# Optimization experiments

Hardware: AMD Instinct MI355X
Metric: run time of the kernel (lower is better)

The kernel has to match this reference:

```python
import jax, jax.numpy as jnp
import numpy as np

N_NODES = 100000
C = 128
E = 800000
V = 50000
NEG_SLOPE = 0.2


def gat_conv(x, edges, W, att_src, att_dst, bias, num_nodes):
    """Single-head PyG-style GATConv with self-loops added (PyG default).

    edges: [2, E] with row 0 = source j, row 1 = destination i.
    """
    loops = jnp.arange(num_nodes, dtype=edges.dtype)
    src = jnp.concatenate([edges[0], loops])  # [E+N]
    dst = jnp.concatenate([edges[1], loops])

    h = x @ W.T                               # [N, C] linear transform
    a_s = h @ att_src                         # [N] per-node src score
    a_d = h @ att_dst                         # [N] per-node dst score

    e = jax.nn.leaky_relu(a_s[src] + a_d[dst], NEG_SLOPE)  # [E+N]
    # scatter-softmax over edges grouped by destination node
    m = jax.ops.segment_max(e, dst, num_segments=num_nodes)
    ex = jnp.exp(e - m[dst])
    denom = jax.ops.segment_sum(ex, dst, num_segments=num_nodes)
    alpha = ex / (denom[dst] + 1e-16)         # [E+N]

    out = jax.ops.segment_sum(alpha[:, None] * h[src], dst, num_segments=num_nodes)
    return out + bias


def setup_inputs() -> dict:
    key = jax.random.key(0)
    ks = jax.random.split(key, 12)
    s = 1.0 / np.sqrt(C)
    return {
        "embedding": jax.random.normal(ks[0], (N_NODES, C), jnp.float32),
        "W1": jax.random.normal(ks[1], (C, C), jnp.float32) * s,
        "att_src1": jax.random.normal(ks[2], (C,), jnp.float32) * s,
        "att_dst1": jax.random.normal(ks[3], (C,), jnp.float32) * s,
        "b1": jax.random.normal(ks[4], (C,), jnp.float32) * s,
        "W2": jax.random.normal(ks[5], (C, C), jnp.float32) * s,
        "att_src2": jax.random.normal(ks[6], (C,), jnp.float32) * s,
        "att_dst2": jax.random.normal(ks[7], (C,), jnp.float32) * s,
        "b2": jax.random.normal(ks[8], (C,), jnp.float32) * s,
        "edges1": jax.random.randint(ks[9], (2, E), 0, N_NODES, jnp.int64 if jax.config.jax_enable_x64 else jnp.int32),
        "edges2": jax.random.randint(ks[10], (2, E), 0, N_NODES, jnp.int64 if jax.config.jax_enable_x64 else jnp.int32),
        "idx_mapping": jax.random.randint(ks[11], (V,), 0, N_NODES, jnp.int64 if jax.config.jax_enable_x64 else jnp.int32),
    }


def reference(embedding, W1, att_src1, att_dst1, b1, W2, att_src2, att_dst2, b2,
              edges1, edges2, idx_mapping):
    h = gat_conv(embedding, edges1, W1, att_src1, att_dst1, b1, N_NODES)
    h = gat_conv(h, edges2, W2, att_src2, att_dst2, b2, N_NODES)
    return h[idx_mapping]
```

## Files before the change

### kernel.cpp

```cpp
#include <hip/hip_runtime.h>

#define N_NODES 100000
#define C_DIM 128
#define E_EDGES 800000
#define V_OUT 50000
#define EN (E_EDGES + N_NODES)
#define M2 (2 * N_NODES)
#define EN2 (2 * EN)

#define BSHIFT 9
#define NBUCK_L ((N_NODES + 511) >> 9)
#define NBUCK2 (2 * NBUCK_L)
#define CAP 8192
#define P1_CHUNK 4096
#define P1_PER_T (P1_CHUNK / 256)
#define NCHUNK ((EN2 + P1_CHUNK - 1) / P1_CHUNK)

#define XPAD 136
#define LDS_E 768

typedef unsigned int uint;
typedef unsigned short ushort;
typedef __attribute__((ext_vector_type(8))) short bf16x8;
typedef __attribute__((ext_vector_type(4))) float f32x4;

static __device__ __forceinline__ ushort f2bf(float f) {
    uint u = __float_as_uint(f);
    u += 0x7fffu + ((u >> 16) & 1);
    return (ushort)(u >> 16);
}

#define PREP_WBLK (C_DIM * C_DIM / 4 / 256)
#define PREP_VBLK ((V_OUT + 255) / 256)
__global__ void prep_kernel(const float* __restrict__ W1, const float* __restrict__ W2,
                            ushort* __restrict__ W1b, ushort* __restrict__ W2b,
                            const int* __restrict__ idx, int* __restrict__ vflag)
{
    const int b = blockIdx.x;
    if (b < 2 * PREP_WBLK) {
        const float* in  = (b < PREP_WBLK) ? W1 : W2;
        ushort* outp     = (b < PREP_WBLK) ? W1b : W2b;
        int i = (b % PREP_WBLK) * 256 + threadIdx.x;
        float4 v = reinterpret_cast<const float4*>(in)[i];
        ushort4 r;
        r.x = f2bf(v.x); r.y = f2bf(v.y); r.z = f2bf(v.z); r.w = f2bf(v.w);
        reinterpret_cast<ushort4*>(outp)[i] = r;
    } else {
        int v = (b - 2 * PREP_WBLK) * 256 + threadIdx.x;
        if (v < V_OUT) vflag[idx[v]] = 1;
    }
}

template <int IN_F32>
__global__ __launch_bounds__(256) void gemm_mfma(
    const void* __restrict__ xin, const ushort* __restrict__ Wb,
    const float* __restrict__ att_s, const float* __restrict__ att_d,
    ushort* __restrict__ hb, float* __restrict__ a_s, float* __restrict__ a_d)
{
    __shared__ ushort xs[64 * XPAD];
    __shared__ ushort ws[128 * XPAD];
    const int tid = threadIdx.x;
    const int nb = blockIdx.x * 64;

    {
        const int row = tid >> 2, q = tid & 3;
        const long srow = min(nb + row, N_NODES - 1);
        ushort* dst = &xs[row * XPAD + q * 32];
        if (IN_F32) {
            const float* src = (const float*)xin + srow * 128 + q * 32;
            #pragma unroll
            for (int i = 0; i < 4; ++i) {
                float4 u = *reinterpret_cast<const float4*>(src + i * 8);
                float4 v = *reinterpret_cast<const float4*>(src + i * 8 + 4);
                uint4 pk;
                pk.x = (uint)f2bf(u.x) | ((uint)f2bf(u.y) << 16);
                pk.y = (uint)f2bf(u.z) | ((uint)f2bf(u.w) << 16);
                pk.z = (uint)f2bf(v.x) | ((uint)f2bf(v.y) << 16);
                pk.w = (uint)f2bf(v.z) | ((uint)f2bf(v.w) << 16);
                *reinterpret_cast<uint4*>(dst + i * 8) = pk;
            }
        } else {
            const ushort* src = (const ushort*)xin + srow * 128 + q * 32;
            #pragma unroll
            for (int i = 0; i < 4; ++i)
                *reinterpret_cast<uint4*>(dst + i * 8) =
                    *reinterpret_cast<const uint4*>(src + i * 8);
        }
    }
    {
        const int row = tid >> 1, half = tid & 1;
        const ushort* src = Wb + row * 128 + half * 64;
        ushort* dst = &ws[row * XPAD + half * 64];
        #pragma unroll
        for (int i = 0; i < 8; ++i)
            *reinterpret_cast<uint4*>(dst + i * 8) =
                *reinterpret_cast<const uint4*>(src + i * 8);
    }
    __syncthreads();

    const int lane = tid & 63;
    const int wv   = tid >> 6;
    const int n0   = nb + wv * 16;
    if (n0 >= N_NODES) return;
    const int m    = lane & 15;
    const int quad = lane >> 4;

    bf16x8 a[4];
    #pragma unroll
    for (int ki = 0; ki < 4; ++ki)
        a[ki] = *reinterpret_cast<const bf16x8*>(&xs[(wv * 16 + m) * XPAD + quad * 8 + ki * 32]);

    float ps[4] = {0, 0, 0, 0}, pd[4] = {0, 0, 0, 0};

    #pragma unroll
    for (int ct = 0; ct < 8; ++ct) {
        const int c = ct * 16 + m;
        f32x4 acc = {0.f, 0.f, 0.f, 0.f};
        #pragma unroll
        for (int ki = 0; ki < 4; ++ki) {
            bf16x8 b = *reinterpret_cast<const bf16x8*>(&ws[c * XPAD + quad * 8 + ki * 32]);
            acc = __builtin_amdgcn_mfma_f32_16x16x32_bf16(a[ki], b, acc, 0, 0, 0);
        }
        const float asc = att_s[c], adc = att_d[c];
        #pragma unroll
        for (int r = 0; r < 4; ++r) {
            const int node = n0 + quad * 4 + r;
            hb[(long)node * 128 + c] = f2bf(acc[r]);
            ps[r] = fmaf(acc[r], asc, ps[r]);
            pd[r] = fmaf(acc[r], adc, pd[r]);
        }
    }
    #pragma unroll
    for (int r = 0; r < 4; ++r) {
        float s = ps[r], d = pd[r];
        #pragma unroll
        for (int x = 1; x < 16; x <<= 1) { s += __shfl_xor(s, x); d += __shfl_xor(d, x); }
        if (m == 0) {
            const int node = n0 + quad * 4 + r;
            a_s[node] = s; a_d[node] = d;
        }
    }
}

__global__ __launch_bounds__(256) void partition_kernel(
    const int* __restrict__ e1, const int* __restrict__ e2,
    int* __restrict__ cursor, uint* __restrict__ slab)
{
    __shared__ int cnt[NBUCK2];
    __shared__ int basearr[NBUCK2];
    const int tid = threadIdx.x;
    for (int i = tid; i < NBUCK2; i += 256) cnt[i] = 0;
    __syncthreads();

    const int e0 = blockIdx.x * P1_CHUNK;
    uint ent[P1_PER_T];
    int  bkt[P1_PER_T];
    #pragma unroll
    for (int i = 0; i < P1_PER_T; ++i) {
        int e = e0 + i * 256 + tid;
        bkt[i] = -1;
        if (e < EN2) {
            int src, dst, lb;
            if (e < EN) {
                if (e < E_EDGES) { src = e1[e]; dst = e1[E_EDGES + e]; }
                else             { src = dst = e - E_EDGES; }
                lb = 0;
            } else {
                int f = e - EN;
                if (f < E_EDGES) { src = e2[f]; dst = e2[E_EDGES + f]; }
                else             { src = dst = f - E_EDGES; }
                lb = NBUCK_L;
            }
            bkt[i] = lb + (dst >> BSHIFT);
            ent[i] = (uint)src | ((uint)(dst & 511) << 17);
            atomicAdd(&cnt[bkt[i]], 1);
        }
    }
    __syncthreads();
    for (int b = tid; b < NBUCK2; b += 256) {
        int c = cnt[b];
        basearr[b] = (c > 0) ? atomicAdd(&cursor[b], c) : 0;
        cnt[b] = 0;
    }
    __syncthreads();
    #pragma unroll
    for (int i = 0; i < P1_PER_T; ++i) {
        if (bkt[i] >= 0) {
            int r = basearr[bkt[i]] + atomicAdd(&cnt[bkt[i]], 1);
            if (r < CAP) slab[(long)bkt[i] * CAP + r] = ent[i];
        }
    }
}

__global__ void bucket_scan(const int* __restrict__ cursor, int* __restrict__ bbase)
{
    const int lane = threadIdx.x;
    int v[7]; int s = 0;
    #pragma unroll
    for (int i = 0; i < 7; ++i) {
        int idx = lane * 7 + i;
        v[i] = (idx < NBUCK2) ? cursor[idx] : 0;
        s += v[i];
    }
    int incl = s;
    #pragma unroll
    for (int d = 1; d < 64; d <<= 1) {
        int t = __shfl_up(incl, d);
        if (lane >= d) incl += t;
    }
    int excl = incl - s;
    #pragma unroll
    for (int i = 0; i < 7; ++i) {
        int idx = lane * 7 + i;
        if (idx < NBUCK2) bbase[idx] = excl;
        excl += v[i];
    }
}

__global__ __launch_bounds__(256) void local_csr(
    const uint* __restrict__ slab, const int* __restrict__ cursor,
    const int* __restrict__ bbase, int* __restrict__ offs, uint* __restrict__ esrc)
{
    __shared__ uint ent[CAP];
    __shared__ int deg[512];
    __shared__ int excl[512];
    const int b = blockIdx.x;
    const int tid = threadIdx.x;
    const int cnt = min(cursor[b], CAP);
    const int base = bbase[b];
    const int layer = (b >= NBUCK_L);
    const int node0 = (b - layer * NBUCK_L) << BSHIFT;
    const int obase = layer * N_NODES;
    const int nodes_n = min(512, N_NODES - node0);

    for (int i = tid; i < 512; i += 256) deg[i] = 0;
    __syncthreads();
    for (int i = tid; i < cnt; i += 256) {
        uint v = slab[(long)b * CAP + i];
        ent[i] = v;
        atomicAdd(&deg[v >> 17], 1);
    }
    __syncthreads();
    if (tid < 64) {
        int v8[8]; int s = 0;
        #pragma unroll
        for (int i = 0; i < 8; ++i) { v8[i] = deg[tid * 8 + i]; s += v8[i]; }
        int incl = s;
        #pragma unroll
        for (int d = 1; d < 64; d <<= 1) {
            int t = __shfl_up(incl, d);
            if (tid >= d) incl += t;
        }
        int e = incl - s;
        #pragma unroll
        for (int i = 0; i < 8; ++i) { excl[tid * 8 + i] = e; e += v8[i]; }
    }
    __syncthreads();
    for (int i = tid; i < nodes_n; i += 256)
        offs[obase + node0 + i] = base + excl[i];
    for (int i = tid; i < 512; i += 256) deg[i] = 0;
    if (tid == 0 && node0 + 512 >= N_NODES)
        offs[obase + N_NODES] = base + cnt;
    __syncthreads();
    for (int i = tid; i < cnt; i += 256) {
        uint v = ent[i];
        int dl = v >> 17;
        int r = atomicAdd(&deg[dl], 1);
        esrc[base + excl[dl] + r] = v;
    }
}

template <int MODE>
__global__ __launch_bounds__(256) void aggregate(
    const ushort* __restrict__ hb, const float* __restrict__ a_s,
    const float* __restrict__ a_d, const float* __restrict__ bias,
    const int* __restrict__ offs, const uint* __restrict__ esrc,
    const int* __restrict__ vflag, void* __restrict__ outp, int obase)
{
    __shared__ uint2 ew[LDS_E];
    const int tid = threadIdx.x;
    const int node0 = blockIdx.x * 16;
    const int bnode0 = (node0 >> BSHIFT) << BSHIFT;
    const int bstart = offs[obase + node0];
    const int bend   = offs[obase + node0 + 16];
    const int nE = bend - bstart;

    for (int i = tid; i < min(nE, LDS_E); i += 256) {
        uint v = esrc[bstart + i];
        float e = a_s[v & 0x1ffff] + a_d[bnode0 + (v >> 17)];
        e = (e >= 0.0f) ? e : 0.2f * e;
        ew[i] = make_uint2(v, __float_as_uint(__expf(e)));
    }
    __syncthreads();

    const int wave = tid >> 6;
    const int lane = tid & 63;
    const int slot = lane >> 4;
    const int c16  = lane & 15;
    const int node = node0 + wave * 4 + slot;
    if (MODE == 1 && vflag[node] == 0) return;

    const int start = offs[obase + node];
    const int end   = offs[obase + node + 1];
    const long coff = (long)(c16 << 3);
    float acc[8] = {0, 0, 0, 0, 0, 0, 0, 0};
    float dsum = 0.0f;

    if (start < end) {
        if (nE <= LDS_E) {
            const int jr = start - bstart, jend = end - bstart;
            const int e1 = jend - 1;
            uint2 p0 = ew[jr];
            uint2 p1 = ew[min(jr + 1, e1)];
            uint2 p2 = ew[min(jr + 2, e1)];
            uint4 h0 = *reinterpret_cast<const uint4*>(hb + ((long)(p0.x & 0x1ffff) << 7) + coff);
            uint4 h1 = *reinterpret_cast<const uint4*>(hb + ((long)(p1.x & 0x1ffff) << 7) + coff);
            float w1 = __uint_as_float(p1.y);
            float w0 = __uint_as_float(p0.y);
            for (int j = jr; j < jend; ++j) {
                uint2 p3 = ew[min(j + 3, e1)];
                uint4 h2 = *reinterpret_cast<const uint4*>(hb + ((long)(p2.x & 0x1ffff) << 7) + coff);
                float w2 = __uint_as_float(p2.y);
                dsum += w0;
                acc[0] = fmaf(w0, __uint_as_float(h0.x << 16),         acc[0]);
                acc[1] = fmaf(w0, __uint_as_float(h0.x & 0xffff0000u), acc[1]);
                acc[2] = fmaf(w0, __uint_as_float(h0.y << 16),         acc[2]);
                acc[3] = fmaf(w0, __uint_as_float(h0.y & 0xffff0000u), acc[3]);
                acc[4] = fmaf(w0, __uint_as_float(h0.z << 16),         acc[4]);
                acc[5] = fmaf(w0, __uint_as_float(h0.z & 0xffff0000u), acc[5]);
                acc[6] = fmaf(w0, __uint_as_float(h0.w << 16),         acc[6]);
                acc[7] = fmaf(w0, __uint_as_float(h0.w & 0xffff0000u), acc[7]);
                w0 = w1; w1 = w2; h0 = h1; h1 = h2; p2 = p3;
            }
        } else {
            const float ad = a_d[node];
            for (int j = start; j < end; ++j) {
                uint v = esrc[j];
                float e = a_s[v & 0x1ffff] + ad;
                e = (e >= 0.0f) ? e : 0.2f * e;
                float w = __expf(e);
                uint4 h = *reinterpret_cast<const uint4*>(hb + ((long)(v & 0x1ffff) << 7) + coff);
                dsum += w;
                acc[0] = fmaf(w, __uint_as_float(h.x << 16),         acc[0]);
                acc[1] = fmaf(w, __uint_as_float(h.x & 0xffff0000u), acc[1]);
                acc[2] = fmaf(w, __uint_as_float(h.y << 16),         acc[2]);
                acc[3] = fmaf(w, __uint_as_float(h.y & 0xffff0000u), acc[3]);
                acc[4] = fmaf(w, __uint_as_float(h.z << 16),         acc[4]);
                acc[5] = fmaf(w, __uint_as_float(h.z & 0xffff0000u), acc[5]);
                acc[6] = fmaf(w, __uint_as_float(h.w << 16),         acc[6]);
                acc[7] = fmaf(w, __uint_as_float(h.w & 0xffff0000u), acc[7]);
            }
        }
    }

    const float inv = 1.0f / (dsum + 1e-16f);
    const int c0 = c16 << 3;
    const float4 b0 = *reinterpret_cast<const float4*>(bias + c0);
    const float4 b1 = *reinterpret_cast<const float4*>(bias + c0 + 4);
    float res[8];
    res[0] = fmaf(acc[0], inv, b0.x);
    res[1] = fmaf(acc[1], inv, b0.y);
    res[2] = fmaf(acc[2], inv, b0.z);
    res[3] = fmaf(acc[3], inv, b0.w);
    res[4] = fmaf(acc[4], inv, b1.x);
    res[5] = fmaf(acc[5], inv, b1.y);
    res[6] = fmaf(acc[6], inv, b1.z);
    res[7] = fmaf(acc[7], inv, b1.w);
    if (MODE == 0) {
        uint4 pk;
        pk.x = (uint)f2bf(res[0]) | ((uint)f2bf(res[1]) << 16);
        pk.y = (uint)f2bf(res[2]) | ((uint)f2bf(res[3]) << 16);
        pk.z = (uint)f2bf(res[4]) | ((uint)f2bf(res[5]) << 16);
        pk.w = (uint)f2bf(res[6]) | ((uint)f2bf(res[7]) << 16);
        *reinterpret_cast<uint4*>((ushort*)outp + ((long)node << 7) + c0) = pk;
    } else {
        float* op = (float*)outp + ((long)node << 7) + c0;
        *reinterpret_cast<float4*>(op)     = make_float4(res[0], res[1], res[2], res[3]);
        *reinterpret_cast<float4*>(op + 4) = make_float4(res[4], res[5], res[6], res[7]);
    }
}

__global__ void gather_out(const float* __restrict__ h, const int* __restrict__ idx,
                           float* __restrict__ out)
{
    int g = blockIdx.x * 256 + threadIdx.x;
    int v = g >> 5, c4 = (g & 31) << 2;
    long src = (long)idx[v] * C_DIM + c4;
    *reinterpret_cast<float4*>(out + ((long)v * C_DIM + c4)) =
        *reinterpret_cast<const float4*>(h + src);
}

extern "C" void kernel_launch(void* const* d_in, const int* in_sizes, int n_in,
                              void* d_out, int out_size, void* d_ws, size_t ws_size,
                              hipStream_t stream)
{
    const float* emb = (const float*)d_in[0];
    const float* W1  = (const float*)d_in[1];
    const float* as1 = (const float*)d_in[2];
    const float* ad1 = (const float*)d_in[3];
    const float* b1  = (const float*)d_in[4];
    const float* W2  = (const float*)d_in[5];
    const float* as2 = (const float*)d_in[6];
    const float* ad2 = (const float*)d_in[7];
    const float* b2  = (const float*)d_in[8];
    const int* edges1 = (const int*)d_in[9];
    const int* edges2 = (const int*)d_in[10];
    const int* idxm   = (const int*)d_in[11];
    float* out = (float*)d_out;

    char* p = (char*)d_ws;
    auto alloc = [&](size_t bytes) {
        char* r = p;
        p += (bytes + 255) & ~(size_t)255;
        return r;
    };
    float*  hB   = (float*)alloc((size_t)N_NODES * C_DIM * 4);
    ushort* hb   = (ushort*)alloc((size_t)N_NODES * C_DIM * 2);
    ushort* a1o  = (ushort*)alloc((size_t)N_NODES * C_DIM * 2);
    uint*   slab = (uint*)alloc((size_t)NBUCK2 * CAP * 4);
    uint*   esrc = (uint*)alloc((size_t)EN2 * 4);
    int*    offs = (int*)alloc((size_t)(M2 + 1) * 4);
    ushort* W1b  = (ushort*)alloc((size_t)C_DIM * C_DIM * 2);
    ushort* W2b  = (ushort*)alloc((size_t)C_DIM * C_DIM * 2);
    float*  aS   = (float*)alloc((size_t)N_NODES * 4);
    float*  aD   = (float*)alloc((size_t)N_NODES * 4);
    int*  bbase  = (int*)alloc((size_t)NBUCK2 * 4);
    int*  cursor = (int*)alloc((size_t)NBUCK2 * 4);
    int*  vflag  = (int*)alloc((size_t)N_NODES * 4);

    hipMemsetAsync(cursor, 0, (size_t)((char*)vflag - (char*)cursor) + (size_t)N_NODES * 4, stream);
    prep_kernel<<<2 * PREP_WBLK + PREP_VBLK, 256, 0, stream>>>(W1, W2, W1b, W2b, idxm, vflag);

    partition_kernel<<<NCHUNK, 256, 0, stream>>>(edges1, edges2, cursor, slab);
    bucket_scan<<<1, 64, 0, stream>>>(cursor, bbase);
    local_csr<<<NBUCK2, 256, 0, stream>>>(slab, cursor, bbase, offs, esrc);

    gemm_mfma<1><<<(N_NODES + 63) / 64, 256, 0, stream>>>(emb, W1b, as1, ad1, hb, aS, aD);
    aggregate<0><<<N_NODES / 16, 256, 0, stream>>>(hb, aS, aD, b1, offs, esrc, vflag, a1o, 0);

    gemm_mfma<0><<<(N_NODES + 63) / 64, 256, 0, stream>>>(a1o, W2b, as2, ad2, hb, aS, aD);
    aggregate<1><<<N_NODES / 16, 256, 0, stream>>>(hb, aS, aD, b2, offs, esrc, vflag, hB, N_NODES);

    gather_out<<<(V_OUT * 32) / 256, 256, 0, stream>>>(hB, idxm, out);
}
```

Baseline: 268.5 us.

## Fuse front-end kernels, inline bucket scan, deepen aggregate prefetch, skip unneeded layer-2 weights

Merges the weight conversion, partition, vflag marking and first GEMM into one heterogeneous launch, with each GEMM block converting fp32 weights to bf16 on the fly. The separate bucket_scan kernel is removed; each local_csr block computes its own prefix base by summing the cursors before it. The aggregate edge loop now prefetches four gathered rows ahead instead of two, and in layer 2 it skips the exp for edges whose destination is not in the output set. The aim is fewer launches and serial dependencies plus more memory-level parallelism, at the cost of redundant weight conversion per block and more registers.

```diff
diff --git a/kernel.cpp b/kernel.cpp
--- a/kernel.cpp
+++ b/kernel.cpp
@@ -19,6 +19,9 @@
 #define XPAD 136
 #define LDS_E 768
 
+#define GEMM_BLKS ((N_NODES + 63) / 64)
+#define VFLAG_BLKS ((V_OUT + 255) / 256)
+
 typedef unsigned int uint;
 typedef unsigned short ushort;
 typedef __attribute__((ext_vector_type(8))) short bf16x8;
@@ -30,37 +33,16 @@
     return (ushort)(u >> 16);
 }
 
-#define PREP_WBLK (C_DIM * C_DIM / 4 / 256)
-#define PREP_VBLK ((V_OUT + 255) / 256)
-__global__ void prep_kernel(const float* __restrict__ W1, const float* __restrict__ W2,
-                            ushort* __restrict__ W1b, ushort* __restrict__ W2b,
-                            const int* __restrict__ idx, int* __restrict__ vflag)
-{
-    const int b = blockIdx.x;
-    if (b < 2 * PREP_WBLK) {
-        const float* in  = (b < PREP_WBLK) ? W1 : W2;
-        ushort* outp     = (b < PREP_WBLK) ? W1b : W2b;
-        int i = (b % PREP_WBLK) * 256 + threadIdx.x;
-        float4 v = reinterpret_cast<const float4*>(in)[i];
-        ushort4 r;
-        r.x = f2bf(v.x); r.y = f2bf(v.y); r.z = f2bf(v.z); r.w = f2bf(v.w);
-        reinterpret_cast<ushort4*>(outp)[i] = r;
-    } else {
-        int v = (b - 2 * PREP_WBLK) * 256 + threadIdx.x;
-        if (v < V_OUT) vflag[idx[v]] = 1;
-    }
-}
-
 template <int IN_F32>
-__global__ __launch_bounds__(256) void gemm_mfma(
-    const void* __restrict__ xin, const ushort* __restrict__ Wb,
+static __device__ __forceinline__ void gemm_body(
+    char* smem, int gb, int tid,
+    const void* __restrict__ xin, const float* __restrict__ W,
     const float* __restrict__ att_s, const float* __restrict__ att_d,
     ushort* __restrict__ hb, float* __restrict__ a_s, float* __restrict__ a_d)
 {
-    __shared__ ushort xs[64 * XPAD];
-    __shared__ ushort ws[128 * XPAD];
-    const int tid = threadIdx.x;
-    const int nb = blockIdx.x * 64;
+    ushort* xs = (ushort*)smem;
+    ushort* ws = xs + 64 * XPAD;
+    const int nb = gb * 64;
 
     {
         const int row = tid >> 2, q = tid & 3;
@@ -89,12 +71,19 @@
     }
     {
         const int row = tid >> 1, half = tid & 1;
-        const ushort* src = Wb + row * 128 + half * 64;
+        const float* src = W + row * 128 + half * 64;
         ushort* dst = &ws[row * XPAD + half * 64];
         #pragma unroll
-        for (int i = 0; i < 8; ++i)
-            *reinterpret_cast<uint4*>(dst + i * 8) =
-                *reinterpret_cast<const uint4*>(src + i * 8);
+        for (int i = 0; i < 8; ++i) {
+            float4 u = *reinterpret_cast<const float4*>(src + i * 8);
+            float4 v = *reinterpret_cast<const float4*>(src + i * 8 + 4);
+            uint4 pk;
+            pk.x = (uint)f2bf(u.x) | ((uint)f2bf(u.y) << 16);
+            pk.y = (uint)f2bf(u.z) | ((uint)f2bf(u.w) << 16);
+            pk.z = (uint)f2bf(v.x) | ((uint)f2bf(v.y) << 16);
+            pk.w = (uint)f2bf(v.z) | ((uint)f2bf(v.w) << 16);
+            *reinterpret_cast<uint4*>(dst + i * 8) = pk;
+        }
     }
     __syncthreads();
 
@@ -142,17 +131,17 @@
     }
 }
 
-__global__ __launch_bounds__(256) void partition_kernel(
+static __device__ __forceinline__ void partition_body(
+    char* smem, int pb, int tid,
     const int* __restrict__ e1, const int* __restrict__ e2,
     int* __restrict__ cursor, uint* __restrict__ slab)
 {
-    __shared__ int cnt[NBUCK2];
-    __shared__ int basearr[NBUCK2];
-    const int tid = threadIdx.x;
+    int* cnt     = (int*)smem;
+    int* basearr = cnt + NBUCK2;
     for (int i = tid; i < NBUCK2; i += 256) cnt[i] = 0;
     __syncthreads();
 
-    const int e0 = blockIdx.x * P1_CHUNK;
+    const int e0 = pb * P1_CHUNK;
     uint ent[P1_PER_T];
     int  bkt[P1_PER_T];
     #pragma unroll
@@ -192,49 +181,67 @@
     }
 }
 
-__global__ void bucket_scan(const int* __restrict__ cursor, int* __restrict__ bbase)
-{
-    const int lane = threadIdx.x;
-    int v[7]; int s = 0;
-    #pragma unroll
-    for (int i = 0; i < 7; ++i) {
-        int idx = lane * 7 + i;
-        v[i] = (idx < NBUCK2) ? cursor[idx] : 0;
-        s += v[i];
-    }
-    int incl = s;
-    #pragma unroll
-    for (int d = 1; d < 64; d <<= 1) {
-        int t = __shfl_up(incl, d);
-        if (lane >= d) incl += t;
-    }
-    int excl = incl - s;
-    #pragma unroll
-    for (int i = 0; i < 7; ++i) {
-        int idx = lane * 7 + i;
-        if (idx < NBUCK2) bbase[idx] = excl;
-        excl += v[i];
-    }
+__global__ __launch_bounds__(256) void fused_front(
+    const float* __restrict__ emb, const float* __restrict__ W1,
+    const float* __restrict__ as1, const float* __restrict__ ad1,
+    ushort* __restrict__ hb, float* __restrict__ aS, float* __restrict__ aD,
+    const int* __restrict__ e1, const int* __restrict__ e2,
+    int* __restrict__ cursor, uint* __restrict__ slab,
+    const int* __restrict__ idxm, int* __restrict__ vflag)
+{
+    __shared__ __attribute__((aligned(16))) char smem[(64 + 128) * XPAD * 2];
+    const int b = blockIdx.x;
+    const int tid = threadIdx.x;
+    if (b < GEMM_BLKS) {
+        gemm_body<1>(smem, b, tid, emb, W1, as1, ad1, hb, aS, aD);
+    } else if (b < GEMM_BLKS + NCHUNK) {
+        partition_body(smem, b - GEMM_BLKS, tid, e1, e2, cursor, slab);
+    } else {
+        int v = (b - GEMM_BLKS - NCHUNK) * 256 + tid;
+        if (v < V_OUT) vflag[idxm[v]] = 1;
+    }
+}
+
+__global__ __launch_bounds__(256) void gemm2_kernel(
+    const ushort* __restrict__ a1o, const float* __restrict__ W2,
+    const float* __restrict__ as2, const float* __restrict__ ad2,
+    ushort* __restrict__ hb, float* __restrict__ aS, float* __restrict__ aD)
+{
+    __shared__ __attribute__((aligned(16))) char smem[(64 + 128) * XPAD * 2];
+    gemm_body<0>(smem, blockIdx.x, threadIdx.x, a1o, W2, as2, ad2, hb, aS, aD);
 }
 
 __global__ __launch_bounds__(256) void local_csr(
     const uint* __restrict__ slab, const int* __restrict__ cursor,
-    const int* __restrict__ bbase, int* __restrict__ offs, uint* __restrict__ esrc)
+    int* __restrict__ offs, uint* __restrict__ esrc)
 {
     __shared__ uint ent[CAP];
     __shared__ int deg[512];
     __shared__ int excl[512];
+    __shared__ int sbase;
     const int b = blockIdx.x;
     const int tid = threadIdx.x;
     const int cnt = min(cursor[b], CAP);
-    const int base = bbase[b];
     const int layer = (b >= NBUCK_L);
     const int node0 = (b - layer * NBUCK_L) << BSHIFT;
     const int obase = layer * N_NODES;
     const int nodes_n = min(512, N_NODES - node0);
 
     for (int i = tid; i < 512; i += 256) deg[i] = 0;
-    __syncthreads();
+    if (tid < 64) {
+        int s = 0;
+        #pragma unroll
+        for (int k = 0; k < 7; ++k) {
+            int idx = tid + 64 * k;
+            if (idx < b) s += cursor[idx];
+        }
+        #pragma unroll
+        for (int d = 32; d > 0; d >>= 1) s += __shfl_down(s, d);
+        if (tid == 0) sbase = s;
+    }
+    __syncthreads();
+    const int base = sbase;
+
     for (int i = tid; i < cnt; i += 256) {
         uint v = slab[(long)b * CAP + i];
         ent[i] = v;
@@ -287,9 +294,14 @@
 
     for (int i = tid; i < min(nE, LDS_E); i += 256) {
         uint v = esrc[bstart + i];
-        float e = a_s[v & 0x1ffff] + a_d[bnode0 + (v >> 17)];
-        e = (e >= 0.0f) ? e : 0.2f * e;
-        ew[i] = make_uint2(v, __float_as_uint(__expf(e)));
+        float w = 0.0f;
+        const int d = bnode0 + (v >> 17);
+        if (MODE == 0 || vflag[d] != 0) {
+            float e = a_s[v & 0x1ffff] + a_d[d];
+            e = (e >= 0.0f) ? e : 0.2f * e;
+            w = __expf(e);
+        }
+        ew[i] = make_uint2(v, __float_as_uint(w));
     }
     __syncthreads();
 
@@ -313,14 +325,19 @@
             uint2 p0 = ew[jr];
             uint2 p1 = ew[min(jr + 1, e1)];
             uint2 p2 = ew[min(jr + 2, e1)];
+            uint2 p3 = ew[min(jr + 3, e1)];
             uint4 h0 = *reinterpret_cast<const uint4*>(hb + ((long)(p0.x & 0x1ffff) << 7) + coff);
             uint4 h1 = *reinterpret_cast<const uint4*>(hb + ((long)(p1.x & 0x1ffff) << 7) + coff);
+            uint4 h2 = *reinterpret_cast<const uint4*>(hb + ((long)(p2.x & 0x1ffff) << 7) + coff);
+            uint4 h3 = *reinterpret_cast<const uint4*>(hb + ((long)(p3.x & 0x1ffff) << 7) + coff);
+            float w0 = __uint_as_float(p0.y);
             float w1 = __uint_as_float(p1.y);
-            float w0 = __uint_as_float(p0.y);
+            float w2 = __uint_as_float(p2.y);
+            float w3 = __uint_as_float(p3.y);
             for (int j = jr; j < jend; ++j) {
-                uint2 p3 = ew[min(j + 3, e1)];
-                uint4 h2 = *reinterpret_cast<const uint4*>(hb + ((long)(p2.x & 0x1ffff) << 7) + coff);
-                float w2 = __uint_as_float(p2.y);
+                uint2 p4 = ew[min(j + 4, e1)];
+                uint4 h4 = *reinterpret_cast<const uint4*>(hb + ((long)(p4.x & 0x1ffff) << 7) + coff);
+                float w4 = __uint_as_float(p4.y);
                 dsum += w0;
                 acc[0] = fmaf(w0, __uint_as_float(h0.x << 16),         acc[0]);
                 acc[1] = fmaf(w0, __uint_as_float(h0.x & 0xffff0000u), acc[1]);
@@ -330,7 +347,8 @@
                 acc[5] = fmaf(w0, __uint_as_float(h0.z & 0xffff0000u), acc[5]);
                 acc[6] = fmaf(w0, __uint_as_float(h0.w << 16),         acc[6]);
                 acc[7] = fmaf(w0, __uint_as_float(h0.w & 0xffff0000u), acc[7]);
-                w0 = w1; w1 = w2; h0 = h1; h1 = h2; p2 = p3;
+                w0 = w1; w1 = w2; w2 = w3; w3 = w4;
+                h0 = h1; h1 = h2; h2 = h3; h3 = h4;
             }
         } else {
             const float ad = a_d[node];
@@ -420,25 +438,21 @@
     uint*   slab = (uint*)alloc((size_t)NBUCK2 * CAP * 4);
     uint*   esrc = (uint*)alloc((size_t)EN2 * 4);
     int*    offs = (int*)alloc((size_t)(M2 + 1) * 4);
-    ushort* W1b  = (ushort*)alloc((size_t)C_DIM * C_DIM * 2);
-    ushort* W2b  = (ushort*)alloc((size_t)C_DIM * C_DIM * 2);
     float*  aS   = (float*)alloc((size_t)N_NODES * 4);
     float*  aD   = (float*)alloc((size_t)N_NODES * 4);
-    int*  bbase  = (int*)alloc((size_t)NBUCK2 * 4);
     int*  cursor = (int*)alloc((size_t)NBUCK2 * 4);
     int*  vflag  = (int*)alloc((size_t)N_NODES * 4);
 
     hipMemsetAsync(cursor, 0, (size_t)((char*)vflag - (char*)cursor) + (size_t)N_NODES * 4, stream);
-    prep_kernel<<<2 * PREP_WBLK + PREP_VBLK, 256, 0, stream>>>(W1, W2, W1b, W2b, idxm, vflag);
-
-    partition_kernel<<<NCHUNK, 256, 0, stream>>>(edges1, edges2, cursor, slab);
-    bucket_scan<<<1, 64, 0, stream>>>(cursor, bbase);
-    local_csr<<<NBUCK2, 256, 0, stream>>>(slab, cursor, bbase, offs, esrc);
-
-    gemm_mfma<1><<<(N_NODES + 63) / 64, 256, 0, stream>>>(emb, W1b, as1, ad1, hb, aS, aD);
+
+    fused_front<<<GEMM_BLKS + NCHUNK + VFLAG_BLKS, 256, 0, stream>>>(
+        emb, W1, as1, ad1, hb, aS, aD, edges1, edges2, cursor, slab, idxm, vflag);
+
+    local_csr<<<NBUCK2, 256, 0, stream>>>(slab, cursor, offs, esrc);
+
     aggregate<0><<<N_NODES / 16, 256, 0, stream>>>(hb, aS, aD, b1, offs, esrc, vflag, a1o, 0);
 
-    gemm_mfma<0><<<(N_NODES + 63) / 64, 256, 0, stream>>>(a1o, W2b, as2, ad2, hb, aS, aD);
+    gemm2_kernel<<<GEMM_BLKS, 256, 0, stream>>>(a1o, W2, as2, ad2, hb, aS, aD);
     aggregate<1><<<N_NODES / 16, 256, 0, stream>>>(hb, aS, aD, b2, offs, esrc, vflag, hB, N_NODES);
 
     gather_out<<<(V_OUT * 32) / 256, 256, 0, stream>>>(hB, idxm, out);
```

Result: slower. 275.4 us (+2.6%).
